# Kernel optimization log

Hardware: AMD Instinct MI355X
Metric: run time of the kernel (lower is better)

Reference implementation:

```python
import jax, jax.numpy as jnp
import numpy as np

DIM = 512
H = 8
HD = DIM // H
MAX_DIST = 128
TABLE = (2 * MAX_DIST + 1) ** 2
LAMBDA_INIT = 0.8


def setup_inputs() -> dict:
    key = jax.random.key(0)
    ks = jax.random.split(key, 20)
    B, Nq, Nkv = 4, 1024, 1024
    inp = {
        "x_q": jax.random.normal(ks[0], (B, Nq, DIM), jnp.float32),
        "x_kv": jax.random.normal(ks[1], (B, Nkv, DIM), jnp.float32),
        "coords_q": jax.random.randint(ks[2], (B, Nq, 2), 0, 256, jnp.int32),
        "coords_k": jax.random.randint(ks[3], (B, Nkv, 2), 0, 256, jnp.int32),
        "alpha_map": jax.random.uniform(ks[4], (B, Nq, 1), jnp.float32),
        "Wq": jax.random.normal(ks[5], (DIM, DIM), jnp.float32) * 0.02,
        "bq": jnp.zeros((DIM,), jnp.float32),
        "Wk": jax.random.normal(ks[6], (DIM, DIM), jnp.float32) * 0.02,
        "bk": jnp.zeros((DIM,), jnp.float32),
        "Wv": jax.random.normal(ks[7], (DIM, DIM), jnp.float32) * 0.02,
        "bv": jnp.zeros((DIM,), jnp.float32),
        "lambda_q1": jax.random.normal(ks[8], (H // 2, HD), jnp.float32) * 0.1,
        "lambda_k1": jax.random.normal(ks[9], (H // 2, HD), jnp.float32) * 0.1,
        "lambda_q2": jax.random.normal(ks[10], (H // 2, HD), jnp.float32) * 0.1,
        "lambda_k2": jax.random.normal(ks[11], (H // 2, HD), jnp.float32) * 0.1,
        "rpe_table": jax.random.normal(ks[12], (TABLE, H), jnp.float32) * 0.02,
        "Wp": jax.random.normal(ks[13], (DIM, DIM), jnp.float32) * 0.02,
        "bp": jnp.zeros((DIM,), jnp.float32),
    }
    return inp


def reference(x_q, x_kv, coords_q, coords_k, alpha_map,
              Wq, bq, Wk, bk, Wv, bv,
              lambda_q1, lambda_k1, lambda_q2, lambda_k2,
              rpe_table, Wp, bp):
    B, Nq, C = x_q.shape
    Nkv = x_kv.shape[1]
    n_half = H // 2
    scale = HD ** -0.5

    # projections -> [B, H, N, HD]
    q = (x_q @ Wq.T + bq).reshape(B, Nq, H, HD).transpose(0, 2, 1, 3)
    k = (x_kv @ Wk.T + bk).reshape(B, Nkv, H, HD).transpose(0, 2, 1, 3)
    v = (x_kv @ Wv.T + bv).reshape(B, Nkv, H, HD).transpose(0, 2, 1, 3)

    # sparse relative position bias: gather per-pair from table
    rel = coords_q[:, :, None, :] - coords_k[:, None, :, :] + MAX_DIST  # [B,Nq,Nkv,2]
    rel = jnp.clip(rel, 0, 2 * MAX_DIST)
    idx = rel[..., 0] * (2 * MAX_DIST + 1) + rel[..., 1]  # [B,Nq,Nkv]
    bias = rpe_table[idx].transpose(0, 3, 1, 2)  # [B,H,Nq,Nkv]

    scores = jnp.einsum('bhqd,bhkd->bhqk', q, k) * scale + bias
    probs = jax.nn.softmax(scores, axis=-1)
    x_std = jnp.einsum('bhqk,bhkd->bhqd', probs, v)

    lam1 = jnp.exp(jnp.sum(lambda_q1 * lambda_k1, axis=-1))  # [n_half]
    lam2 = jnp.exp(jnp.sum(lambda_q2 * lambda_k2, axis=-1))
    lam = (lam1 - lam2 + LAMBDA_INIT)[None, :, None, None]

    attn_diff = probs[:, :n_half] - lam * probs[:, n_half:]
    x_diff = jnp.einsum('bhqk,bhkd->bhqd', attn_diff, v[:, :n_half])

    alpha = alpha_map[:, None]  # [B,1,Nq,1]
    x1 = x_std[:, :n_half] + alpha * x_diff
    x = jnp.concatenate([x1, x_std[:, n_half:]], axis=1)  # [B,H,Nq,HD]
    x = x.transpose(0, 2, 1, 3).reshape(B, Nq, C)
    return x @ Wp.T + bp
```

## Files before the change

kernel.cpp:

```cpp
#include <hip/hip_runtime.h>
#include <cstddef>
#include <cstdint>

#define DIM   512
#define NSEQ  1024
#define NB    4
#define LOG2E 1.44269504f
#define TBL8  528392

typedef unsigned short u16;
typedef short bf16x8 __attribute__((ext_vector_type(8)));
typedef _Float16 half8v __attribute__((ext_vector_type(8)));
typedef float f32x4  __attribute__((ext_vector_type(4)));

#define MFMA(a, b, c)  __builtin_amdgcn_mfma_f32_16x16x32_bf16(a, b, c, 0, 0, 0)
#define MFMAH(a, b, c) __builtin_amdgcn_mfma_f32_16x16x32_f16(a, b, c, 0, 0, 0)

__device__ inline void split2(float x, u16& h, u16& l) {
  unsigned u = __float_as_uint(x);
  unsigned hb = (u + 0x7fffu + ((u >> 16) & 1u)) >> 16;
  float fh = __uint_as_float(hb << 16);
  float r = x - fh;
  unsigned v = __float_as_uint(r);
  unsigned lb = (v + 0x7fffu + ((v >> 16) & 1u)) >> 16;
  h = (u16)hb; l = (u16)lb;
}

__device__ inline uint2 pack4(const u16 a[4]) {
  return make_uint2((unsigned)a[0] | ((unsigned)a[1] << 16),
                    (unsigned)a[2] | ((unsigned)a[3] << 16));
}

__device__ inline u16 f2h(float x) {
  _Float16 h = (_Float16)x;
  u16 r; __builtin_memcpy(&r, &h, 2);
  return r;
}
__device__ inline float h2f(u16 b) {
  _Float16 h; __builtin_memcpy(&h, &b, 2);
  return (float)h;
}
__device__ inline unsigned pkh2(float a, float b) {
  return (unsigned)f2h(a) | ((unsigned)f2h(b) << 16);
}

__device__ inline void split_body(const float* __restrict__ in,
                                  u16* __restrict__ out, int e4) {
  const int e = e4 * 4;
  const int m = e >> 9, c = e & 511;
  const float4 v = *(const float4*)(in + e);
  u16 h[4], l[4];
  split2(v.x, h[0], l[0]); split2(v.y, h[1], l[1]);
  split2(v.z, h[2], l[2]); split2(v.w, h[3], l[3]);
  u16* o = out + (size_t)m * 1024 + c;
  *(uint2*)o = pack4(h);
  *(uint2*)(o + 512) = pack4(l);
}

#define GLDS(g, l)                                                        \
  __builtin_amdgcn_global_load_lds(                                       \
      (const __attribute__((address_space(1))) void*)(g),                 \
      (__attribute__((address_space(3))) void*)(l), 16, 0, 0)

__global__ __launch_bounds__(256) void prep_split(
    const float* __restrict__ wq, const float* __restrict__ wk,
    const float* __restrict__ wv, const float* __restrict__ wp,
    const float* __restrict__ xq, const float* __restrict__ xkv,
    const float* __restrict__ rpe,
    u16* __restrict__ w2, u16* __restrict__ xq2, u16* __restrict__ xkv2,
    u16* __restrict__ rpe16) {
  const int id = blockIdx.x;
  const int t = threadIdx.x;
  if (id < 1024) {
    const int y = id >> 8;
    const float* src = (y == 0) ? wq : (y == 1) ? wk : (y == 2) ? wv : wp;
    split_body(src, w2 + (size_t)y * 524288, (id & 255) * 256 + t);
  } else if (id < 5120) {
    const int e = id - 1024;
    const int y = e >> 11;
    split_body(y ? xkv : xq, y ? xkv2 : xq2, (e & 2047) * 256 + t);
  } else {
    const int e = (id - 5120) * 2048 + t * 8;
    if (e < TBL8) {
      const float4 f0 = *(const float4*)(rpe + e);
      const float4 f1 = *(const float4*)(rpe + e + 4);
      uint4 o;
      o.x = pkh2(f0.x * LOG2E, f0.y * LOG2E);
      o.y = pkh2(f0.z * LOG2E, f0.w * LOG2E);
      o.z = pkh2(f1.x * LOG2E, f1.y * LOG2E);
      o.w = pkh2(f1.z * LOG2E, f1.w * LOG2E);
      *(uint4*)(rpe16 + e) = o;
    }
  }
}

template <int OUT_MODE>
__device__ __forceinline__ void gemm_db(
    u16 (*__restrict__ As)[8192], u16 (*__restrict__ Bs)[8192],
    const u16* __restrict__ A2, const u16* __restrict__ B2,
    const float* __restrict__ bias, void* __restrict__ outp,
    float scale, int m0, int n0) {
  const int tid = threadIdx.x;
  const int lane = tid & 63, w = tid >> 6;
  const int wm = (w & 1) * 64, wn = (w >> 1) * 64;
  const int lr8 = lane >> 3;
  const int scc = (lane & 7) ^ lr8;
  const int colA = ((scc & 3) * 8) + ((scc >> 2) * 512);

  const int fr = lane & 15, kq = lane >> 4, fx = fr & 7;
  int aoh[4], aol[4], boh[4], bol[4];
#pragma unroll
  for (int i = 0; i < 4; ++i) {
    const int ra = (wm + i * 16 + fr) * 64;
    aoh[i] = ra + ((kq ^ fx)) * 8;
    aol[i] = ra + (((4 + kq) ^ fx)) * 8;
    const int rb = (wn + i * 16 + fr) * 64;
    boh[i] = rb + ((kq ^ fx)) * 8;
    bol[i] = rb + (((4 + kq) ^ fx)) * 8;
  }

  auto stage = [&](int it, int p) {
    const int k0 = it * 32;
#pragma unroll
    for (int i = 0; i < 4; ++i) {
      const int rA = m0 + w * 32 + i * 8 + lr8;
      GLDS(A2 + (size_t)rA * 1024 + colA + k0,
           (char*)As[p] + (w * 32 + i * 8) * 128);
      const int rB = n0 + w * 32 + i * 8 + lr8;
      GLDS(B2 + (size_t)rB * 1024 + colA + k0,
           (char*)Bs[p] + (w * 32 + i * 8) * 128);
    }
  };

  f32x4 acc[4][4] = {};
  stage(0, 0);
  for (int it = 0; it < 16; ++it) {
    const int p = it & 1;
    __syncthreads();
    if (it + 1 < 16) stage(it + 1, p ^ 1);
    const u16* Ab = As[p];
    const u16* Bb = Bs[p];
    bf16x8 ah[4], al[4], bh[4], bl[4];
#pragma unroll
    for (int i = 0; i < 4; ++i) {
      ah[i] = *(const bf16x8*)(Ab + aoh[i]);
      al[i] = *(const bf16x8*)(Ab + aol[i]);
      bh[i] = *(const bf16x8*)(Bb + boh[i]);
      bl[i] = *(const bf16x8*)(Bb + bol[i]);
    }
#pragma unroll
    for (int i = 0; i < 4; ++i)
#pragma unroll
      for (int j = 0; j < 4; ++j) {
        acc[i][j] = MFMA(al[i], bh[j], acc[i][j]);
        acc[i][j] = MFMA(ah[i], bl[j], acc[i][j]);
        acc[i][j] = MFMA(ah[i], bh[j], acc[i][j]);
      }
  }

  const int er = (lane >> 4) * 4, ec = lane & 15;
#pragma unroll
  for (int i = 0; i < 4; ++i)
#pragma unroll
    for (int j = 0; j < 4; ++j) {
      const int row = m0 + wm + i * 16 + er;
      const int col = n0 + wn + j * 16 + ec;
      const float bv = bias[col];
      if (OUT_MODE == 4) {
        u16 hf[4];
#pragma unroll
        for (int r = 0; r < 4; ++r) hf[r] = f2h((acc[i][j][r] + bv) * scale);
        const int bb = row >> 10, kk = row & 1023;
        *(uint2*)((u16*)outp + ((size_t)(bb * 512 + col)) * 1024 + kk) =
            pack4(hf);
      } else {
#pragma unroll
        for (int r = 0; r < 4; ++r)
          ((u16*)outp)[(size_t)(row + r) * 512 + col] =
              f2h((acc[i][j][r] + bv) * scale);
      }
    }
}

__global__ __launch_bounds__(256) void qkv_rpe(
    const u16* __restrict__ xq2, const u16* __restrict__ xkv2,
    const u16* __restrict__ w2, const float* __restrict__ bq,
    const float* __restrict__ bk, const float* __restrict__ bv,
    u16* __restrict__ q2f, u16* __restrict__ k2f, u16* __restrict__ vtf,
    const int* __restrict__ cq, const int* __restrict__ ck,
    const u16* __restrict__ rpe16, u16* __restrict__ biasT) {
  __shared__ __align__(16) u16 As[2][8192], Bs[2][8192];
  const int id = blockIdx.x;
  const int t = threadIdx.x;
  if (id < 384) {
    const int z = id >> 7, rem = id & 127;
    const int m0 = (rem & 31) * 128, n0 = (rem >> 5) * 128;
    if (z == 0)
      gemm_db<3>(As, Bs, xq2, w2, bq, q2f, 0.125f * LOG2E, m0, n0);
    else if (z == 1)
      gemm_db<3>(As, Bs, xkv2, w2 + 524288, bk, k2f, 1.0f, m0, n0);
    else
      gemm_db<4>(As, Bs, xkv2, w2 + 2 * 524288, bv, vtf, 1.0f, m0, n0);
  } else {
    const int e = id - 384;
    const int q0 = (e & 15) * 64, k0 = ((e >> 4) & 63) * 16, b = e >> 10;
    const int qn = t & 63, kb = t >> 6;
    const int2 cqv = ((const int2*)cq)[b * NSEQ + q0 + qn];
    uint4 g[4];
#pragma unroll
    for (int j = 0; j < 4; ++j) {
      const int k = kb * 4 + j;
      const int2 ckv = ((const int2*)ck)[b * NSEQ + k0 + k];
      const int r0 = min(max(cqv.x - ckv.x + 128, 0), 256);
      const int r1 = min(max(cqv.y - ckv.y + 128, 0), 256);
      g[j] = *(const uint4*)(rpe16 + (size_t)(r0 * 257 + r1) * 8);
    }
    u16* dst0 = biasT + ((size_t)(b * 8) << 20) + q0 + qn;
#pragma unroll
    for (int j = 0; j < 4; ++j) {
      u16* dst = dst0 + ((size_t)(k0 + kb * 4 + j) << 10);
      const unsigned ww[4] = {g[j].x, g[j].y, g[j].z, g[j].w};
#pragma unroll
      for (int p2 = 0; p2 < 4; ++p2) {
        dst[(size_t)(2 * p2 + 0) << 20] = (u16)(ww[p2] & 0xffffu);
        dst[(size_t)(2 * p2 + 1) << 20] = (u16)(ww[p2] >> 16);
      }
    }
  }
}

__global__ __launch_bounds__(256, 3) void gemm_out(
    const u16* __restrict__ A2, const u16* __restrict__ B2,
    const float* __restrict__ bias, float* __restrict__ out) {
  __shared__ __align__(16) u16 Ah[8192], Al[8192], Bh[4096], Bl[4096];
  const int m0 = blockIdx.x * 128, n0 = blockIdx.y * 64;
  const int tid = threadIdx.x;
  const int lane = tid & 63, w = tid >> 6;
  const int wm = (w & 1) * 64, wn = (w >> 1) * 32;
  const int lr = lane >> 3;
  const int scc = (lane & 7) ^ lr;

  const u16* gA = A2 + (size_t)(m0 + w * 32 + lr) * 1024 + scc * 8;
  const u16* gB = B2 + (size_t)(n0 + w * 16 + lr) * 1024 + scc * 8;
  char* lAh = (char*)Ah + w * 4096;  char* lAl = (char*)Al + w * 4096;
  char* lBh = (char*)Bh + w * 2048;  char* lBl = (char*)Bl + w * 2048;

  const int fr = lane & 15, kq = lane >> 4, fx = fr & 7;
  int aoff[2][4], boff[2][2];
#pragma unroll
  for (int s = 0; s < 2; ++s) {
#pragma unroll
    for (int i = 0; i < 4; ++i)
      aoff[s][i] = (wm + i * 16 + fr) * 64 + (((s * 4 + kq) ^ fx)) * 8;
#pragma unroll
    for (int j = 0; j < 2; ++j)
      boff[s][j] = (wn + j * 16 + fr) * 64 + (((s * 4 + kq) ^ fx)) * 8;
  }

  f32x4 acc[4][2] = {};
  for (int k0 = 0; k0 < 512; k0 += 64) {
    __syncthreads();
#pragma unroll
    for (int i = 0; i < 4; ++i) {
      GLDS(gA + (size_t)i * 8192 + k0, lAh + i * 1024);
      GLDS(gA + (size_t)i * 8192 + 512 + k0, lAl + i * 1024);
    }
#pragma unroll
    for (int i = 0; i < 2; ++i) {
      GLDS(gB + (size_t)i * 8192 + k0, lBh + i * 1024);
      GLDS(gB + (size_t)i * 8192 + 512 + k0, lBl + i * 1024);
    }
    __syncthreads();
#pragma unroll
    for (int s = 0; s < 2; ++s) {
      bf16x8 ah[4], al[4], bh[2], bl[2];
#pragma unroll
      for (int i = 0; i < 4; ++i) {
        ah[i] = *(const bf16x8*)(Ah + aoff[s][i]);
        al[i] = *(const bf16x8*)(Al + aoff[s][i]);
      }
#pragma unroll
      for (int j = 0; j < 2; ++j) {
        bh[j] = *(const bf16x8*)(Bh + boff[s][j]);
        bl[j] = *(const bf16x8*)(Bl + boff[s][j]);
      }
#pragma unroll
      for (int i = 0; i < 4; ++i)
#pragma unroll
        for (int j = 0; j < 2; ++j) {
          acc[i][j] = MFMA(al[i], bh[j], acc[i][j]);
          acc[i][j] = MFMA(ah[i], bl[j], acc[i][j]);
          acc[i][j] = MFMA(ah[i], bh[j], acc[i][j]);
        }
    }
  }

  const int er = (lane >> 4) * 4, ec = lane & 15;
#pragma unroll
  for (int i = 0; i < 4; ++i)
#pragma unroll
    for (int j = 0; j < 2; ++j) {
      const int row = m0 + wm + i * 16 + er;
      const int col = n0 + wn + j * 16 + ec;
      const float bv = bias[col];
#pragma unroll
      for (int r = 0; r < 4; ++r)
        out[(size_t)(row + r) * 512 + col] = acc[i][j][r] + bv;
    }
}

__global__ __launch_bounds__(512) void attn_f16(
    const u16* __restrict__ q2f, const u16* __restrict__ k2f,
    const u16* __restrict__ vtf, const float* __restrict__ amap,
    const float* __restrict__ lq1, const float* __restrict__ lk1,
    const float* __restrict__ lq2, const float* __restrict__ lk2,
    const u16* __restrict__ biasT, u16* __restrict__ xo) {
  __shared__ __align__(16) u16 KsL[2][2][4096];
  __shared__ __align__(16) u16 VtL[2][2][4096];
  __shared__ float2 mls[2][2][2][16];
  __shared__ float l2s[32];
  __shared__ float lam_s;

  const int tid = threadIdx.x;
  const int lane = tid & 63, w = tid >> 6;
  const int kg = w >> 2, h = (w >> 1) & 1, qs = w & 1;
  const int wl = w & 3;
  const int hp = blockIdx.y, b = blockIdx.z;
  const int q0 = blockIdx.x * 32;
  const int head = hp + 4 * h;
  const int lq = lane & 15, lg = lane >> 4;
  const int q = qs * 16 + lq;
  const size_t qrow = (size_t)(b * NSEQ + q0 + q);

  if (tid < 64) {
    float p1 = lq1[hp * 64 + tid] * lk1[hp * 64 + tid];
    float p2 = lq2[hp * 64 + tid] * lk2[hp * 64 + tid];
#pragma unroll
    for (int m = 32; m >= 1; m >>= 1) {
      p1 += __shfl_xor(p1, m, 64);
      p2 += __shfl_xor(p2, m, 64);
    }
    if (tid == 0) lam_s = __expf(p1) - __expf(p2) + 0.8f;
  }

  const float alpha = amap[qrow];

  half8v Qf[2];
#pragma unroll
  for (int ks = 0; ks < 2; ++ks)
    Qf[ks] = *(const half8v*)(q2f + qrow * 512 + head * 64 + ks * 32 + lg * 8);

  f32x4 Ya[4] = {};
  f32x4 Yb[4] = {};
  float m_run = -1e30f, l_run = 0.0f;

  const int lr = lane >> 3;
  const int lc = (lane & 7) ^ lr;
  const int cw = wl * 2;

  auto stage = [&](int it, int p) {
    const int kbase = kg * 512 + it * 32;
#pragma unroll
    for (int i = 0; i < 2; ++i) {
      const int c = cw + i;
      const int row = c * 8 + lr;
      const int sh = row >> 5, k = row & 31;
      const u16* src = k2f + (size_t)(b * NSEQ + kbase + k) * 512 +
                       (hp + 4 * sh) * 64 + lc * 8;
      GLDS(src, (char*)KsL[kg][p] + c * 1024);
    }
#pragma unroll
    for (int i = 0; i < 2; ++i) {
      const int c = cw + i;
      const int d = c * 8 + lr;
      const int hv = lc >> 2, kc = lc & 3;
      const u16* src = vtf + (size_t)(b * 512 + (hp + 4 * hv) * 64 + d) * 1024 +
                       kbase + kc * 8;
      GLDS(src, (char*)VtL[kg][p] + c * 1024);
    }
  };

  const u16* bT = biasT + ((size_t)(b * 8 + head) << 20) + q0 + q;

  stage(0, 0);

  for (int it = 0; it < 16; ++it) {
    const int p = it & 1;
    __syncthreads();
    if (it + 1 < 16) stage(it + 1, p ^ 1);

    u16 rb[8];
    {
      const u16* bt = bT + (size_t)(kg * 512 + it * 32) * 1024;
#pragma unroll
      for (int kt = 0; kt < 2; ++kt)
#pragma unroll
        for (int r = 0; r < 4; ++r)
          rb[kt * 4 + r] = bt[(size_t)(kt * 16 + lg * 4 + r) * 1024];
    }

    const u16* Kb = KsL[kg][p];
    f32x4 st[2] = {};
#pragma unroll
    for (int kt = 0; kt < 2; ++kt) {
      const int krow = kt * 16 + lq;
      const int rx = krow & 7;
#pragma unroll
      for (int ks = 0; ks < 2; ++ks) {
        const int phys = (ks * 4 + lg) ^ rx;
        const half8v kf = *(const half8v*)(Kb + (h * 32 + krow) * 64 + phys * 8);
        st[kt] = MFMAH(kf, Qf[ks], st[kt]);
      }
    }

    float sv[2][4];
    float mx = -1e30f;
#pragma unroll
    for (int kt = 0; kt < 2; ++kt)
#pragma unroll
      for (int r = 0; r < 4; ++r) {
        const float s = st[kt][r] + h2f(rb[kt * 4 + r]);
        sv[kt][r] = s;
        mx = fmaxf(mx, s);
      }
    mx = fmaxf(mx, __shfl_xor(mx, 16, 64));
    mx = fmaxf(mx, __shfl_xor(mx, 32, 64));
    const float mnew = fmaxf(m_run, mx);
    const float a = exp2f(m_run - mnew);
    m_run = mnew;
    float pr[2][4], ps = 0.0f;
#pragma unroll
    for (int kt = 0; kt < 2; ++kt)
#pragma unroll
      for (int r = 0; r < 4; ++r) {
        pr[kt][r] = exp2f(sv[kt][r] - mnew);
        ps += pr[kt][r];
      }
    ps += __shfl_xor(ps, 16, 64);
    ps += __shfl_xor(ps, 32, 64);
    l_run = l_run * a + ps;
#pragma unroll
    for (int dt = 0; dt < 4; ++dt) Ya[dt] *= a;
    if (h == 1) {
#pragma unroll
      for (int dt = 0; dt < 4; ++dt) Yb[dt] *= a;
    }

    const unsigned a0 = pkh2(pr[0][0], pr[0][1]);
    const unsigned a1 = pkh2(pr[0][2], pr[0][3]);
    const unsigned b0 = pkh2(pr[1][0], pr[1][1]);
    const unsigned b1 = pkh2(pr[1][2], pr[1][3]);
    const int srcA = lq + ((lg & 1) << 5);
    const unsigned A0 = __shfl((int)a0, srcA),      A1 = __shfl((int)a1, srcA);
    const unsigned B0 = __shfl((int)b0, srcA),      B1 = __shfl((int)b1, srcA);
    const unsigned C0 = __shfl((int)a0, srcA + 16), C1 = __shfl((int)a1, srcA + 16);
    const unsigned D0 = __shfl((int)b0, srcA + 16), D1 = __shfl((int)b1, srcA + 16);
    const bool t2 = lg >= 2;
    const uint4 Pu = make_uint4(t2 ? B0 : A0, t2 ? B1 : A1,
                                t2 ? D0 : C0, t2 ? D1 : C1);
    half8v pb;
    __builtin_memcpy(&pb, &Pu, 16);

    const u16* Vb = VtL[kg][p];
    if (h == 0) {
#pragma unroll
      for (int dt = 0; dt < 4; ++dt) {
        const int d = dt * 16 + lq;
        const half8v v1 = *(const half8v*)(Vb + d * 64 + ((lg ^ (d & 7))) * 8);
        Ya[dt] = MFMAH(v1, pb, Ya[dt]);
      }
    } else {
#pragma unroll
      for (int dt = 0; dt < 4; ++dt) {
        const int d = dt * 16 + lq;
        const int dx = d & 7;
        const half8v v1 = *(const half8v*)(Vb + d * 64 + ((lg ^ dx)) * 8);
        Yb[dt] = MFMAH(v1, pb, Yb[dt]);
        const half8v v2 = *(const half8v*)(Vb + d * 64 + (((4 + lg) ^ dx)) * 8);
        Ya[dt] = MFMAH(v2, pb, Ya[dt]);
      }
    }
  }

  float* mY = (float*)KsL;
  float* mB = (float*)VtL;
  __syncthreads();
  if (lane < 16) mls[kg][h][qs][lane] = make_float2(m_run, l_run);
  if (kg == 1) {
#pragma unroll
    for (int dt = 0; dt < 4; ++dt)
#pragma unroll
      for (int r = 0; r < 4; ++r)
        mY[((h * 2 + qs) * 64 + lane) * 16 + dt * 4 + r] = Ya[dt][r];
    if (h == 1) {
#pragma unroll
      for (int dt = 0; dt < 4; ++dt)
#pragma unroll
        for (int r = 0; r < 4; ++r)
          mB[(qs * 64 + lane) * 16 + dt * 4 + r] = Yb[dt][r];
    }
  }
  __syncthreads();
  float l_tot = l_run;
  if (kg == 0) {
    const float2 o = mls[1][h][qs][lq];
    const float mm = fmaxf(m_run, o.x);
    const float s0 = exp2f(m_run - mm);
    const float s1 = exp2f(o.x - mm);
    l_tot = l_run * s0 + o.y * s1;
    const float* sY = mY + ((h * 2 + qs) * 64 + lane) * 16;
#pragma unroll
    for (int dt = 0; dt < 4; ++dt)
#pragma unroll
      for (int r = 0; r < 4; ++r)
        Ya[dt][r] = Ya[dt][r] * s0 + sY[dt * 4 + r] * s1;
    if (h == 1) {
      const float* sB = mB + (qs * 64 + lane) * 16;
#pragma unroll
      for (int dt = 0; dt < 4; ++dt)
#pragma unroll
        for (int r = 0; r < 4; ++r)
          Yb[dt][r] = Yb[dt][r] * s0 + sB[dt * 4 + r] * s1;
    }
  }

  __syncthreads();
  float* y2x = (float*)KsL;
  if (kg == 0 && h == 1) {
    if (lane < 16) l2s[qs * 16 + lane] = l_tot;
#pragma unroll
    for (int dt = 0; dt < 4; ++dt)
#pragma unroll
      for (int r = 0; r < 4; ++r)
        y2x[(qs * 64 + lane) * 16 + dt * 4 + r] = Yb[dt][r];
  }
  __syncthreads();
  if (kg == 0 && h == 1) {
    const float inv2 = 1.0f / l_tot;
#pragma unroll
    for (int dt = 0; dt < 4; ++dt) {
      u16 hh[4], ll[4];
#pragma unroll
      for (int r = 0; r < 4; ++r) split2(Ya[dt][r] * inv2, hh[r], ll[r]);
      u16* o = xo + qrow * 1024 + (hp + 4) * 64 + dt * 16 + lg * 4;
      *(uint2*)o = pack4(hh);
      *(uint2*)(o + 512) = pack4(ll);
    }
  } else if (kg == 0 && h == 0) {
    const float inv1 = 1.0f / l_tot;
    const float inv2 = 1.0f / l2s[qs * 16 + lq];
    const float c1 = (1.0f + alpha) * inv1;
    const float c2 = alpha * lam_s * inv2;
#pragma unroll
    for (int dt = 0; dt < 4; ++dt) {
      u16 hh[4], ll[4];
#pragma unroll
      for (int r = 0; r < 4; ++r) {
        const float y2 = y2x[(qs * 64 + lane) * 16 + dt * 4 + r];
        split2(c1 * Ya[dt][r] - c2 * y2, hh[r], ll[r]);
      }
      u16* o = xo + qrow * 1024 + hp * 64 + dt * 16 + lg * 4;
      *(uint2*)o = pack4(hh);
      *(uint2*)(o + 512) = pack4(ll);
    }
  }
}

extern "C" void kernel_launch(void* const* d_in, const int* in_sizes, int n_in,
                              void* d_out, int out_size, void* d_ws, size_t ws_size,
                              hipStream_t stream) {
  const float* x_q   = (const float*)d_in[0];
  const float* x_kv  = (const float*)d_in[1];
  const int*   c_q   = (const int*)d_in[2];
  const int*   c_k   = (const int*)d_in[3];
  const float* alpha = (const float*)d_in[4];
  const float* Wq    = (const float*)d_in[5];
  const float* bq    = (const float*)d_in[6];
  const float* Wk    = (const float*)d_in[7];
  const float* bk    = (const float*)d_in[8];
  const float* Wv    = (const float*)d_in[9];
  const float* bv    = (const float*)d_in[10];
  const float* lq1   = (const float*)d_in[11];
  const float* lk1   = (const float*)d_in[12];
  const float* lq2   = (const float*)d_in[13];
  const float* lk2   = (const float*)d_in[14];
  const float* rpe   = (const float*)d_in[15];
  const float* Wp    = (const float*)d_in[16];
  const float* bp    = (const float*)d_in[17];

  u16* w2    = (u16*)d_ws;
  u16* xq2   = (u16*)((char*)d_ws + (4u << 20));
  u16* q2f   = (u16*)((char*)d_ws + (12u << 20));
  u16* k2f   = (u16*)((char*)d_ws + (16u << 20));
  u16* vtf   = (u16*)((char*)d_ws + (20u << 20));
  u16* rpe16 = (u16*)((char*)d_ws + (24u << 20));
  u16* xa    = xq2;
  u16* biasT = (u16*)((char*)d_ws + (28u << 20));
  u16* xkv2  = (u16*)d_out;

  prep_split<<<5379, 256, 0, stream>>>(Wq, Wk, Wv, Wp, x_q, x_kv, rpe,
                                       w2, xq2, xkv2, rpe16);
  qkv_rpe<<<4480, 256, 0, stream>>>(xq2, xkv2, w2, bq, bk, bv,
                                    q2f, k2f, vtf, c_q, c_k, rpe16, biasT);
  attn_f16<<<dim3(32, 4, NB), 512, 0, stream>>>(
      q2f, k2f, vtf, alpha, lq1, lk1, lq2, lk2, biasT, xa);
  gemm_out<<<dim3(32, 8), 256, 0, stream>>>(xa, w2 + 3 * 524288, bp,
                                            (float*)d_out);
}
```

Baseline: 195.2 us.

## Coalesce bias transpose via LDS, prefetch bias, lazy rescale, MFMA priority

The bias-gather blocks now stage their transposed tile in shared memory and write 16-byte coalesced rows to biasT, replacing scattered 2-byte global stores. The attention loop prefetches the next iteration's bias values alongside the K/V staging so their latency overlaps compute. The online-softmax rescale is skipped unless the running max grows by more than 8 (log2 units), which saves multiplies but lets unnormalized probabilities grow up to 2^8 in fp16. s_setprio is raised around the MFMA sections to favour matrix issue.

```diff
diff --git a/kernel.cpp b/kernel.cpp
--- a/kernel.cpp
+++ b/kernel.cpp
@@ -202,6 +202,7 @@
     else
       gemm_db<4>(As, Bs, xkv2, w2 + 2 * 524288, bv, vtf, 1.0f, m0, n0);
   } else {
+    u16* Ts = (u16*)As;
     const int e = id - 384;
     const int q0 = (e & 15) * 64, k0 = ((e >> 4) & 63) * 16, b = e >> 10;
     const int qn = t & 63, kb = t >> 6;
@@ -215,16 +216,26 @@
       const int r1 = min(max(cqv.y - ckv.y + 128, 0), 256);
       g[j] = *(const uint4*)(rpe16 + (size_t)(r0 * 257 + r1) * 8);
     }
-    u16* dst0 = biasT + ((size_t)(b * 8) << 20) + q0 + qn;
 #pragma unroll
     for (int j = 0; j < 4; ++j) {
-      u16* dst = dst0 + ((size_t)(k0 + kb * 4 + j) << 10);
+      const int k = kb * 4 + j;
+      u16* dst = Ts + k * 64 + qn;
       const unsigned ww[4] = {g[j].x, g[j].y, g[j].z, g[j].w};
 #pragma unroll
       for (int p2 = 0; p2 < 4; ++p2) {
-        dst[(size_t)(2 * p2 + 0) << 20] = (u16)(ww[p2] & 0xffffu);
-        dst[(size_t)(2 * p2 + 1) << 20] = (u16)(ww[p2] >> 16);
-      }
+        dst[(2 * p2 + 0) * 1024] = (u16)(ww[p2] & 0xffffu);
+        dst[(2 * p2 + 1) * 1024] = (u16)(ww[p2] >> 16);
+      }
+    }
+    __syncthreads();
+#pragma unroll
+    for (int i = 0; i < 4; ++i) {
+      const int e2 = i * 256 + t;
+      const int row = e2 >> 3, c8 = e2 & 7;
+      const int hh = row >> 4, k = row & 15;
+      const uint4 v = *(const uint4*)(Ts + row * 64 + c8 * 8);
+      *(uint4*)(biasT + ((size_t)(b * 8 + hh) * 1024 + k0 + k) * 1024 +
+                q0 + c8 * 8) = v;
     }
   }
 }
@@ -382,25 +393,31 @@
 
   const u16* bT = biasT + ((size_t)(b * 8 + head) << 20) + q0 + q;
 
+  auto ldbias = [&](int it, u16* r) {
+    const u16* bt = bT + (size_t)(kg * 512 + it * 32) * 1024;
+#pragma unroll
+    for (int kt = 0; kt < 2; ++kt)
+#pragma unroll
+      for (int rr = 0; rr < 4; ++rr)
+        r[kt * 4 + rr] = bt[(size_t)(kt * 16 + lg * 4 + rr) * 1024];
+  };
+
   stage(0, 0);
+  u16 rb[8];
+  ldbias(0, rb);
 
   for (int it = 0; it < 16; ++it) {
     const int p = it & 1;
     __syncthreads();
-    if (it + 1 < 16) stage(it + 1, p ^ 1);
-
-    u16 rb[8];
-    {
-      const u16* bt = bT + (size_t)(kg * 512 + it * 32) * 1024;
-#pragma unroll
-      for (int kt = 0; kt < 2; ++kt)
-#pragma unroll
-        for (int r = 0; r < 4; ++r)
-          rb[kt * 4 + r] = bt[(size_t)(kt * 16 + lg * 4 + r) * 1024];
+    u16 rbn[8];
+    if (it + 1 < 16) {
+      stage(it + 1, p ^ 1);
+      ldbias(it + 1, rbn);
     }
 
     const u16* Kb = KsL[kg][p];
     f32x4 st[2] = {};
+    __builtin_amdgcn_s_setprio(1);
 #pragma unroll
     for (int kt = 0; kt < 2; ++kt) {
       const int krow = kt * 16 + lq;
@@ -412,6 +429,7 @@
         st[kt] = MFMAH(kf, Qf[ks], st[kt]);
       }
     }
+    __builtin_amdgcn_s_setprio(0);
 
     float sv[2][4];
     float mx = -1e30f;
@@ -425,26 +443,29 @@
       }
     mx = fmaxf(mx, __shfl_xor(mx, 16, 64));
     mx = fmaxf(mx, __shfl_xor(mx, 32, 64));
-    const float mnew = fmaxf(m_run, mx);
-    const float a = exp2f(m_run - mnew);
-    m_run = mnew;
+    if (__any(mx > m_run + 8.0f)) {
+      const float mnew = fmaxf(m_run, mx);
+      const float a = exp2f(m_run - mnew);
+      m_run = mnew;
+      l_run *= a;
+#pragma unroll
+      for (int dt = 0; dt < 4; ++dt) Ya[dt] *= a;
+      if (h == 1) {
+#pragma unroll
+        for (int dt = 0; dt < 4; ++dt) Yb[dt] *= a;
+      }
+    }
     float pr[2][4], ps = 0.0f;
 #pragma unroll
     for (int kt = 0; kt < 2; ++kt)
 #pragma unroll
       for (int r = 0; r < 4; ++r) {
-        pr[kt][r] = exp2f(sv[kt][r] - mnew);
+        pr[kt][r] = exp2f(sv[kt][r] - m_run);
         ps += pr[kt][r];
       }
     ps += __shfl_xor(ps, 16, 64);
     ps += __shfl_xor(ps, 32, 64);
-    l_run = l_run * a + ps;
-#pragma unroll
-    for (int dt = 0; dt < 4; ++dt) Ya[dt] *= a;
-    if (h == 1) {
-#pragma unroll
-      for (int dt = 0; dt < 4; ++dt) Yb[dt] *= a;
-    }
+    l_run += ps;
 
     const unsigned a0 = pkh2(pr[0][0], pr[0][1]);
     const unsigned a1 = pkh2(pr[0][2], pr[0][3]);
@@ -462,6 +483,7 @@
     __builtin_memcpy(&pb, &Pu, 16);
 
     const u16* Vb = VtL[kg][p];
+    __builtin_amdgcn_s_setprio(1);
     if (h == 0) {
 #pragma unroll
       for (int dt = 0; dt < 4; ++dt) {
@@ -479,6 +501,12 @@
         const half8v v2 = *(const half8v*)(Vb + d * 64 + (((4 + lg) ^ dx)) * 8);
         Ya[dt] = MFMAH(v2, pb, Ya[dt]);
       }
+    }
+    __builtin_amdgcn_s_setprio(0);
+
+    if (it + 1 < 16) {
+#pragma unroll
+      for (int z = 0; z < 8; ++z) rb[z] = rbn[z];
     }
   }
 
```

After: 196.8 us. No clear change (+0.8%).
